# Performance work log

Hardware: AMD Instinct MI355X
Metric: run time of the kernel (lower is better)

The kernel has to match this reference:

```python
import jax, jax.numpy as jnp
import numpy as np

B, T, IN, H, OUT = 64, 32, 256, 512, 256
M, W, R = 256, 64, 4            # nr_cells, cell_size, read_heads
NN_IN = IN + R * W              # 512
NN_OUT = H + R * W              # 768
IFACE = R * W + 3 * W + 5 * R + 3  # 471
CLIP = 20.0
DELTA = 1e-6


def setup_inputs():
    key = jax.random.key(0)
    ks = jax.random.split(key, 10)
    s = 0.05
    bound = float(np.sqrt(6.0 / (B * H + 2 * H)))  # xavier_uniform on (2,B,H)
    return {
        'x': jax.random.normal(ks[0], (B, T, IN), jnp.float32),
        'h0': jax.random.uniform(ks[1], (2, B, H), jnp.float32, -bound, bound),
        'Wih0': jax.random.normal(ks[2], (4 * H, NN_IN), jnp.float32) * s,
        'Whh0': jax.random.normal(ks[3], (4 * H, H), jnp.float32) * s,
        'bih0': jnp.zeros((4 * H,), jnp.float32),
        'bhh0': jnp.zeros((4 * H,), jnp.float32),
        'Wih1': jax.random.normal(ks[4], (4 * H, H), jnp.float32) * s,
        'Whh1': jax.random.normal(ks[5], (4 * H, H), jnp.float32) * s,
        'bih1': jnp.zeros((4 * H,), jnp.float32),
        'bhh1': jnp.zeros((4 * H,), jnp.float32),
        'Wif': jax.random.normal(ks[6], (IFACE, H), jnp.float32) * s,
        'bif': jnp.zeros((IFACE,), jnp.float32),
        'Wout': jax.random.normal(ks[7], (OUT, NN_OUT), jnp.float32) * s,
        'bout': jnp.zeros((OUT,), jnp.float32),
    }


def _lstm_cell(x, h, c, Wih, Whh, bih, bhh):
    g = x @ Wih.T + bih + h @ Whh.T + bhh
    i, f, gg, o = jnp.split(g, 4, axis=1)  # torch gate order i,f,g,o
    c = jax.nn.sigmoid(f) * c + jax.nn.sigmoid(i) * jnp.tanh(gg)
    h = jax.nn.sigmoid(o) * jnp.tanh(c)
    return h, c


def _content_weights(mem, keys, strengths):
    # mem: (b,M,W), keys: (b,K,W), strengths: (b,K) -> softmax over M
    mem_n = mem / (jnp.linalg.norm(mem, axis=2, keepdims=True) + DELTA)
    key_n = keys / (jnp.linalg.norm(keys, axis=2, keepdims=True) + DELTA)
    sim = jnp.einsum('bkw,bmw->bkm', key_n, mem_n)
    return jax.nn.softmax(sim * strengths[..., None], axis=2)


def _memory_step(xi, mem, link, prec, rw, ww, usage):
    b = xi.shape[0]
    o = 0
    rk = jnp.tanh(xi[:, :R * W].reshape(b, R, W)); o = R * W
    rs = jax.nn.softplus(xi[:, o:o + R]); o += R
    wk = jnp.tanh(xi[:, o:o + W]).reshape(b, 1, W); o += W
    ws = jax.nn.softplus(xi[:, o])[:, None]; o += 1
    ev = jax.nn.sigmoid(xi[:, o:o + W]); o += W
    wv = jnp.tanh(xi[:, o:o + W]); o += W
    fg = jax.nn.sigmoid(xi[:, o:o + R]); o += R
    ag = jax.nn.sigmoid(xi[:, o])[:, None]; o += 1
    wg = jax.nn.sigmoid(xi[:, o])[:, None]; o += 1
    rm = jax.nn.softmax(xi[:, o:o + 3 * R].reshape(b, R, 3), axis=2)

    # usage update (uses OLD read/write weights); single write head
    usage = usage + (1.0 - usage) * ww
    psi = jnp.prod(1.0 - fg[:, :, None] * rw, axis=1)
    usage = usage * psi

    # write content addressing on OLD memory
    wcw = _content_weights(mem, wk, ws)[:, 0]  # (b,M)

    # allocation by ascending sort of usage (exclusive cumprod)
    u = DELTA + (1.0 - DELTA) * usage
    phi = jnp.argsort(u, axis=1)
    sorted_u = jnp.take_along_axis(u, phi, axis=1)
    excl = jnp.cumprod(jnp.concatenate([jnp.ones((b, 1), u.dtype), sorted_u], axis=1), axis=1)[:, :-1]
    sorted_alloc = (1.0 - sorted_u) * excl
    alloc = jnp.take_along_axis(sorted_alloc, jnp.argsort(phi, axis=1), axis=1)

    ww = wg * (ag * alloc + (1.0 - ag) * wcw)  # (b,M)

    # erase + write
    mem = mem * (1.0 - ww[:, :, None] * ev[:, None, :]) + ww[:, :, None] * wv[:, None, :]

    # temporal link matrix + precedence
    prev_scale = 1.0 - ww[:, :, None] - ww[:, None, :]
    link = prev_scale * link + ww[:, :, None] * prec[:, None, :]
    link = link * (1.0 - jnp.eye(M, dtype=link.dtype))
    prec = (1.0 - ww.sum(axis=1, keepdims=True)) * prec + ww

    # read: directional weights use NEW link and OLD read weights; content uses NEW memory
    rcw = _content_weights(mem, rk, rs)               # (b,R,M)
    fwd = jnp.einsum('bij,brj->bri', link, rw)
    bwd = jnp.einsum('brj,bji->bri', rw, link)
    rw = rm[:, :, 0:1] * bwd + rm[:, :, 1:2] * fwd + rm[:, :, 2:3] * rcw
    rvec = jnp.einsum('brm,bmw->brw', rw, mem).reshape(b, R * W)
    return rvec, mem, link, prec, rw, ww, usage


def reference(x, h0, Wih0, Whh0, bih0, bhh0, Wih1, Whh1, bih1, bhh1, Wif, bif, Wout, bout):
    b = x.shape[0]
    lr0 = jnp.zeros((b, R * W), x.dtype)  # initial last_read; NOTE: source concatenates this
    # initial zero last_read to EVERY timestep's controller input (inputs built upfront)
    carry0 = (h0[0], h0[0], h0[1], h0[1],
              jnp.full((b, M, W), DELTA, x.dtype),   # memory
              jnp.zeros((b, M, M), x.dtype),          # link matrix
              jnp.zeros((b, M), x.dtype),             # precedence
              jnp.full((b, R, M), DELTA, x.dtype),    # read weights
              jnp.full((b, M), DELTA, x.dtype),       # write weights
              jnp.zeros((b, M), x.dtype))             # usage

    def step(carry, x_t):
        h0_, c0_, h1_, c1_, mem, link, prec, rw, ww, usage = carry
        inp = jnp.concatenate([x_t, lr0], axis=1)
        h0_, c0_ = _lstm_cell(inp, h0_, c0_, Wih0, Whh0, bih0, bhh0)
        h1_, c1_ = _lstm_cell(h0_, h1_, c1_, Wih1, Whh1, bih1, bhh1)
        out = jnp.clip(h1_, -CLIP, CLIP)
        xi = out @ Wif.T + bif
        rvec, mem, link, prec, rw, ww, usage = _memory_step(xi, mem, link, prec, rw, ww, usage)
        o_t = jnp.concatenate([out, rvec], axis=1)  # (b, NN_OUT)
        return (h0_, c0_, h1_, c1_, mem, link, prec, rw, ww, usage), o_t

    _, ys = jax.lax.scan(step, carry0, jnp.swapaxes(x, 0, 1))  # (T,b,NN_OUT)
    outputs = jnp.tanh(ys) @ Wout.T + bout  # Dropout(p=0) -> Tanh -> Linear
    return jnp.swapaxes(outputs, 0, 1)      # (b,T,OUT)
```

## Files before the change

kernel.cpp:

```cpp
#include <hip/hip_runtime.h>
#include <hip/hip_bf16.h>
#include <math.h>


typedef __bf16 bf16_t;
typedef __attribute__((ext_vector_type(8))) __bf16 bf16x8;
typedef __attribute__((ext_vector_type(4))) float f32x4;

#define B_    64
#define T_    32
#define IN_   256
#define H_    512
#define M_    256
#define W_    64
#define R_    4
#define IFACE_ 471
#define DELTA_ 1e-6f

#define OFF_H0SEQ  (0L)
#define SZ_H0SEQ   (32L*64*512*2)
#define OFF_OUTSEQ (OFF_H0SEQ + SZ_H0SEQ)
#define SZ_OUTSEQ  (32L*64*512*2)
#define OFF_H0BUF  (OFF_OUTSEQ + SZ_OUTSEQ)
#define SZ_HBUF    (2L*64*512*2)
#define OFF_H1BUF  (OFF_H0BUF + SZ_HBUF)
#define OFF_XI     (OFF_H1BUF + SZ_HBUF)
#define SZ_XI      (32L*64*480*4)
#define OFF_RVEC   (OFF_XI + SZ_XI)
#define SZ_RVEC    (32L*64*256*4)
#define OFF_YBF    (OFF_RVEC + SZ_RVEC)
#define SZ_YBF     (32L*64*768*2)
#define OFF_BAR    (OFF_YBF + SZ_YBF)
#define SZ_BAR     (2048L)
#define OFF_XB     (OFF_BAR + SZ_BAR)
#define SZ_XB      (64L*32*256*2)
#define OFF_H0B    (OFF_XB + SZ_XB)
#define SZ_H0B     (2L*64*512*2)
#define OFF_W0     (OFF_H0B + SZ_H0B)
#define SZ_W       (2048L*512*2)
#define OFF_W1     (OFF_W0 + SZ_W)
#define OFF_W2     (OFF_W1 + SZ_W)
#define OFF_W3     (OFF_W2 + SZ_W)
#define OFF_WIF    (OFF_W3 + SZ_W)
#define SZ_WIF     (480L*512*2)
#define OFF_WOUTB  (OFF_WIF + SZ_WIF)
#define SZ_WOUTB   (256L*768*2)
#define OFF_BS0    (OFF_WOUTB + SZ_WOUTB)
#define SZ_BS      (2048L*4)
#define OFF_BS1    (OFF_BS0 + SZ_BS)
#define OFF_BIF    (OFF_BS1 + SZ_BS)
#define SZ_BIF     (2048L)
#define OFF_BOUTF  (OFF_BIF + SZ_BIF)
#define SZ_BOUTF   (1024L)

__device__ __forceinline__ float sigf(float x){ return 1.0f/(1.0f + expf(-x)); }
__device__ __forceinline__ float softplusf(float x){
  return fmaxf(x, 0.0f) + log1pf(expf(-fabsf(x)));
}
__device__ __forceinline__ float wred(float v){
  #pragma unroll
  for (int off = 32; off; off >>= 1) v += __shfl_xor(v, off, 64);
  return v;
}
__device__ __forceinline__ float ldin(const void* p, long i, int mf){
  return mf ? ((const float*)p)[i] : (float)((const bf16_t*)p)[i];
}

__device__ __forceinline__ void treebar64(unsigned* bar, unsigned ps, int bid){
  __syncthreads();
  if (threadIdx.x == 0){
    const unsigned tgt = 8u*(ps + 1u);
    unsigned* cg = bar + ((bid & 7) << 5);
    unsigned a = __hip_atomic_fetch_add(cg, 1u, __ATOMIC_ACQ_REL, __HIP_MEMORY_SCOPE_AGENT);
    if (a == tgt - 1u){
      unsigned b = __hip_atomic_fetch_add(bar + 256, 1u, __ATOMIC_ACQ_REL, __HIP_MEMORY_SCOPE_AGENT);
      if (b == tgt - 1u){
        __hip_atomic_store(bar + 320, ps + 1u, __ATOMIC_RELEASE, __HIP_MEMORY_SCOPE_AGENT);
        __hip_atomic_fetch_add(bar + 288, 1u, __ATOMIC_ACQ_REL, __HIP_MEMORY_SCOPE_AGENT);
      }
    }
    while (__hip_atomic_load(bar + 288, __ATOMIC_ACQUIRE, __HIP_MEMORY_SCOPE_AGENT) < ps + 1u)
      __builtin_amdgcn_s_sleep(1);
  }
  __syncthreads();
}

__global__ void k_detect(const unsigned short* __restrict__ x16,
                         int* __restrict__ flag, unsigned* __restrict__ bar){
  __shared__ int cnt;
  if (threadIdx.x < 8)       bar[threadIdx.x << 5] = 0u;
  else if (threadIdx.x == 8) bar[256] = 0u;
  else if (threadIdx.x == 9) bar[288] = 0u;
  else if (threadIdx.x == 10) bar[320] = 0u;
  if (threadIdx.x == 0) cnt = 0;
  __syncthreads();
  unsigned short u = x16[threadIdx.x * 2];
  int e = (u >> 7) & 0xFF;
  if (e >= 0x88) atomicAdd(&cnt, 1);
  __syncthreads();
  if (threadIdx.x == 0) *flag = (cnt > 16) ? 1 : 0;
}

__global__ void k_convert(const void* x, const void* h0, const void* Wih0,
                          const void* Whh0, const void* bih0, const void* bhh0,
                          const void* Wih1, const void* Whh1, const void* bih1,
                          const void* bhh1, const void* Wif, const void* bif,
                          const void* Wout, const void* bout,
                          bf16_t* __restrict__ xb, bf16_t* __restrict__ h0b,
                          bf16_t* __restrict__ h0buf, bf16_t* __restrict__ h1buf,
                          bf16_t* __restrict__ W0, bf16_t* __restrict__ W1,
                          bf16_t* __restrict__ W2, bf16_t* __restrict__ W3,
                          bf16_t* __restrict__ Wifp, bf16_t* __restrict__ Woutb,
                          float* __restrict__ bs0, float* __restrict__ bs1,
                          float* __restrict__ bifp, float* __restrict__ boutf,
                          const int* __restrict__ flag)
{
  const int mf = *flag;
  const long stride = (long)gridDim.x * blockDim.x;
  long i0 = (long)blockIdx.x * blockDim.x + threadIdx.x;
  switch (blockIdx.y){
  case 0: for (long i = i0; i < 64L*32*256; i += stride) xb[i] = (bf16_t)ldin(x, i, mf); break;
  case 1: for (long i = i0; i < 2L*64*512; i += stride){
            float v = ldin(h0, i, mf); bf16_t bb = (bf16_t)v; h0b[i] = bb;
            if (i < 64*512) h0buf[i] = bb; else h1buf[i - 64*512] = bb;
          } break;
  case 2: for (long i = i0; i < 2048L*512; i += stride) W0[i] = (bf16_t)ldin(Wih0, i, mf); break;
  case 3: for (long i = i0; i < 2048L*512; i += stride) W1[i] = (bf16_t)ldin(Whh0, i, mf); break;
  case 4: for (long i = i0; i < 2048L*512; i += stride) W2[i] = (bf16_t)ldin(Wih1, i, mf); break;
  case 5: for (long i = i0; i < 2048L*512; i += stride) W3[i] = (bf16_t)ldin(Whh1, i, mf); break;
  case 6: for (long i = i0; i < 480L*512; i += stride){
            long r = i >> 9;
            Wifp[i] = (r < IFACE_) ? (bf16_t)ldin(Wif, i, mf) : (bf16_t)0.0f;
          } break;
  case 7: for (long i = i0; i < 256L*768; i += stride) Woutb[i] = (bf16_t)ldin(Wout, i, mf); break;
  case 8:
    for (long i = i0; i < 2048; i += stride){
      bs0[i] = ldin(bih0, i, mf) + ldin(bhh0, i, mf);
      bs1[i] = ldin(bih1, i, mf) + ldin(bhh1, i, mf);
    }
    for (long i = i0; i < 480; i += stride) bifp[i] = (i < IFACE_) ? ldin(bif, i, mf) : 0.0f;
    for (long i = i0; i < 256; i += stride) boutf[i] = ldin(bout, i, mf);
    break;
  }
}

__device__ __forceinline__ void softmax256_wave(float* a, int lane){
  float v0=a[lane], v1=a[64+lane], v2=a[128+lane], v3=a[192+lane];
  float mx = fmaxf(fmaxf(v0,v1), fmaxf(v2,v3));
  #pragma unroll
  for (int off=32; off; off>>=1) mx = fmaxf(mx, __shfl_xor(mx, off, 64));
  v0=expf(v0-mx); v1=expf(v1-mx); v2=expf(v2-mx); v3=expf(v3-mx);
  float s = v0+v1+v2+v3;
  #pragma unroll
  for (int off=32; off; off>>=1) s += __shfl_xor(s, off, 64);
  float inv = 1.0f/s;
  a[lane]=v0*inv; a[64+lane]=v1*inv; a[128+lane]=v2*inv; a[192+lane]=v3*inv;
}

struct ProdShm {
  bf16_t wpool[66560];
  float  cst[64][16];
  float  bias[4][16];
};
struct ConsShm {
  float smem[256][65];
  float xib[480];
  float rkn4r[2][65][4];
  float wkn[64], ev_[64], wvv[64];
  float rs_[4], fg_[4], rm_[4][3];
  float wsS, agS, wgS, wwsumS;
  float invn[256], wcw[256];
  float usage[256], uu[256], su[256], scanA[256];
  int   rank_[256];
  float ww_[256], prec_[256];
  float rw_[4][256];
  float rw4[256][4];
  float fwd_[4][256], bwd_[4][256], rcw_[4][256];
  bf16_t rwb[4][264];
  bf16_t wwb[256], precb[256];
  float p2cT[2][264];
  float p5cT[5][2][264];
  float rvp[8][4][64];
};
union ShUnion { ProdShm p; ConsShm c; };

__global__ __launch_bounds__(512,2) void k_main(
    const bf16_t* __restrict__ xb, const bf16_t* __restrict__ h0b,
    const bf16_t* __restrict__ W0, const bf16_t* __restrict__ W1,
    const bf16_t* __restrict__ W2, const bf16_t* __restrict__ W3,
    const float* __restrict__ bs0, const float* __restrict__ bs1,
    const bf16_t* __restrict__ Wifp, const float* __restrict__ bifp,
    bf16_t* __restrict__ h0buf, bf16_t* __restrict__ h1buf,
    bf16_t* __restrict__ h0seq, bf16_t* __restrict__ outseq,
    float* __restrict__ XI, float* __restrict__ RVEC,
    unsigned* __restrict__ bar)
{
  __shared__ ShUnion sh;
  const int bid = blockIdx.x;
  const int tid = threadIdx.x, lane = tid & 63, wv = tid >> 6;
  const int m16 = lane & 15, q = lane >> 4;

  if (bid < 64){
    ProdShm& P = sh.p;
    const int layer = bid >> 5;
    const int u0 = (bid & 31) * 16;

    if (!layer){
      for (int i = tid; i < 64*32; i += 512){
        int rl = i >> 5, c8 = (i & 31)*8;
        int grow = (rl >> 4)*512 + u0 + (rl & 15);
        *(bf16x8*)&P.wpool[rl*264 + c8] = *(const bf16x8*)(W0 + (size_t)grow*512 + c8);
      }
      for (int i = tid; i < 64*64; i += 512){
        int rl = i >> 6, c8 = (i & 63)*8;
        int grow = (rl >> 4)*512 + u0 + (rl & 15);
        *(bf16x8*)&P.wpool[16896 + rl*520 + c8] = *(const bf16x8*)(W1 + (size_t)grow*512 + c8);
      }
    } else {
      for (int i = tid; i < 64*64; i += 512){
        int rl = i >> 6, c8 = (i & 63)*8;
        int grow = (rl >> 4)*512 + u0 + (rl & 15);
        *(bf16x8*)&P.wpool[rl*520 + c8]         = *(const bf16x8*)(W2 + (size_t)grow*512 + c8);
        *(bf16x8*)&P.wpool[33280 + rl*520 + c8] = *(const bf16x8*)(W3 + (size_t)grow*512 + c8);
      }
    }
    for (int i = tid; i < 64*16; i += 512){
      int b = i >> 4, n = i & 15;
      P.cst[b][n] = (float)h0b[layer*(64*512) + b*512 + u0 + n];
    }
    if (tid < 64){
      int G = tid >> 4, n = tid & 15;
      const float* bs = layer ? bs1 : bs0;
      P.bias[G][n] = bs[G*512 + u0 + n];
    }
    __syncthreads();

    bf16_t* hbuf = layer ? h1buf : h0buf;

    for (int ps = 0; ps <= 33; ++ps){
      if (wv < 4){
        const int t = layer ? (ps - 1) : ps;
        const bool active = layer ? (ps >= 1 && ps <= 32) : (ps < 32);
        if (active){
          const int p = t & 1;
          const bf16_t* hin = hbuf + p*(64*512);
          bf16_t* hout = hbuf + (p^1)*(64*512);
          const int b0 = wv * 16;

          f32x4 acc[4];
          #pragma unroll
          for (int G = 0; G < 4; ++G){ float bv = P.bias[G][m16]; acc[G] = (f32x4){bv,bv,bv,bv}; }

          if (!layer){
            #pragma unroll 2
            for (int kt = 0; kt < 8; ++kt){
              bf16x8 a = *(const bf16x8*)(xb + ((size_t)(b0+m16)*T_ + t)*IN_ + kt*32 + q*8);
              #pragma unroll
              for (int G = 0; G < 4; ++G)
                acc[G] = __builtin_amdgcn_mfma_f32_16x16x32_bf16(
                    a, *(const bf16x8*)&P.wpool[(G*16+m16)*264 + kt*32 + q*8], acc[G], 0, 0, 0);
            }
            #pragma unroll 4
            for (int kt = 0; kt < 16; ++kt){
              bf16x8 a = *(const bf16x8*)(hin + (b0+m16)*512 + kt*32 + q*8);
              #pragma unroll
              for (int G = 0; G < 4; ++G)
                acc[G] = __builtin_amdgcn_mfma_f32_16x16x32_bf16(
                    a, *(const bf16x8*)&P.wpool[16896 + (G*16+m16)*520 + kt*32 + q*8], acc[G], 0, 0, 0);
            }
          } else {
            #pragma unroll 4
            for (int kt = 0; kt < 16; ++kt){
              bf16x8 a = *(const bf16x8*)(h0seq + ((size_t)t*64 + b0+m16)*512 + kt*32 + q*8);
              #pragma unroll
              for (int G = 0; G < 4; ++G)
                acc[G] = __builtin_amdgcn_mfma_f32_16x16x32_bf16(
                    a, *(const bf16x8*)&P.wpool[(G*16+m16)*520 + kt*32 + q*8], acc[G], 0, 0, 0);
            }
            #pragma unroll 4
            for (int kt = 0; kt < 16; ++kt){
              bf16x8 a = *(const bf16x8*)(hin + (b0+m16)*512 + kt*32 + q*8);
              #pragma unroll
              for (int G = 0; G < 4; ++G)
                acc[G] = __builtin_amdgcn_mfma_f32_16x16x32_bf16(
                    a, *(const bf16x8*)&P.wpool[33280 + (G*16+m16)*520 + kt*32 + q*8], acc[G], 0, 0, 0);
            }
          }
          #pragma unroll
          for (int v = 0; v < 4; ++v){
            int b = b0 + q*4 + v;
            float gi = acc[0][v], gf = acc[1][v], gg = acc[2][v], go = acc[3][v];
            float c_ = sigf(gf)*P.cst[b][m16] + sigf(gi)*tanhf(gg);
            P.cst[b][m16] = c_;
            float h = sigf(go)*tanhf(c_);
            bf16_t hb = (bf16_t)h;
            hout[b*512 + u0 + m16] = hb;
            if (!layer) h0seq[((size_t)t*64 + b)*512 + u0 + m16] = hb;
            else        outseq[((size_t)t*64 + b)*512 + u0 + m16] = hb;
          }
        }
      } else if (ps >= 2 && bid < 30){
        const int t2 = ps - 2;
        const int b0 = (wv - 4) * 16;
        const int r = bid*16 + m16;
        float bv = bifp[r];
        f32x4 acc = {bv,bv,bv,bv};
        const bf16_t* arow = outseq + ((size_t)t2*64 + b0 + m16)*512 + q*8;
        const bf16_t* brow = Wifp + (size_t)r*512 + q*8;
        #pragma unroll 4
        for (int kt = 0; kt < 16; ++kt){
          acc = __builtin_amdgcn_mfma_f32_16x16x32_bf16(
              *(const bf16x8*)(arow + kt*32), *(const bf16x8*)(brow + kt*32), acc, 0, 0, 0);
        }
        #pragma unroll
        for (int v = 0; v < 4; ++v)
          XI[((size_t)t2*64 + b0 + q*4 + v)*480 + r] = acc[v];
      }
      treebar64(bar, (unsigned)ps, bid);
    }
  } else {
    ConsShm& S = sh.c;
    const int b = bid - 64;
    const int quad = lane >> 4, li = lane & 15;
    unsigned prog = 0;

    bf16x8 rowL[2][8], colL[2][8];
    #pragma unroll
    for (int g = 0; g < 2; ++g)
      #pragma unroll
      for (int ch = 0; ch < 8; ++ch)
        #pragma unroll
        for (int z = 0; z < 8; ++z){ rowL[g][ch][z] = (bf16_t)0.0f; colL[g][ch][z] = (bf16_t)0.0f; }

    if (tid < 256){
      S.ww_[tid] = DELTA_; S.usage[tid] = 0.0f; S.prec_[tid] = 0.0f;
      S.invn[tid] = 1.0f/(sqrtf(64.0f*DELTA_*DELTA_) + DELTA_);
      S.wwb[tid] = (bf16_t)DELTA_; S.precb[tid] = (bf16_t)0.0f;
      #pragma unroll
      for (int r = 0; r < 4; ++r) S.rw_[r][tid] = DELTA_;
    }
    for (int i = tid; i < 4*264; i += 512) ((bf16_t*)S.rwb)[i] = (bf16_t)DELTA_;
    for (int i = tid; i < 256*65; i += 512) ((float*)S.smem)[i] = DELTA_;
    __syncthreads();

    const int mH = tid >> 1, q2 = tid & 1;

    for (int t = 0; t < 32; ++t){
      if (tid == 0 && prog < (unsigned)(t + 3)){
        for (;;){
          prog = __hip_atomic_load(bar + 320, __ATOMIC_ACQUIRE, __HIP_MEMORY_SCOPE_AGENT);
          if (prog >= (unsigned)(t + 3)) break;
          __builtin_amdgcn_s_sleep(2);
        }
      }
      __syncthreads();
      if (tid < IFACE_) S.xib[tid] = XI[((size_t)t*64 + b)*480 + tid];
      __syncthreads();

      if (wv < 4){
        float v = tanhf(S.xib[wv*64 + lane]);
        float s = wred(v*v);
        float vn = v/(sqrtf(s) + DELTA_);
        S.rkn4r[0][lane][wv] = vn; S.rkn4r[1][lane][wv] = vn;
      } else if (wv == 4){
        float v = tanhf(S.xib[260 + lane]);
        float s = wred(v*v);
        S.wkn[lane] = v/(sqrtf(s) + DELTA_);
      } else if (wv == 5){ S.ev_[lane] = sigf(S.xib[325 + lane]);
      } else if (wv == 6){ S.wvv[lane] = tanhf(S.xib[389 + lane]);
      } else {
        if (lane < 4)        S.rs_[lane] = softplusf(S.xib[256 + lane]);
        else if (lane == 4)  S.wsS = softplusf(S.xib[324]);
        else if (lane < 9)   S.fg_[lane-5] = sigf(S.xib[453 + (lane-5)]);
        else if (lane == 9)  S.agS = sigf(S.xib[457]);
        else if (lane == 10) S.wgS = sigf(S.xib[458]);
        else if (lane >= 16 && lane < 20){
          int r = lane - 16;
          float a0 = S.xib[459+r*3], a1 = S.xib[459+r*3+1], a2 = S.xib[459+r*3+2];
          float mx = fmaxf(a0, fmaxf(a1, a2));
          float e0 = expf(a0-mx), e1 = expf(a1-mx), e2 = expf(a2-mx);
          float s = e0+e1+e2;
          S.rm_[r][0]=e0/s; S.rm_[r][1]=e1/s; S.rm_[r][2]=e2/s;
        }
      }
      __syncthreads();

      if (tid < 256){
        int m = tid;
        float us = S.usage[m] + (1.0f - S.usage[m])*S.ww_[m];
        float psi = (1.0f - S.fg_[0]*S.rw_[0][m]) * (1.0f - S.fg_[1]*S.rw_[1][m])
                  * (1.0f - S.fg_[2]*S.rw_[2][m]) * (1.0f - S.fg_[3]*S.rw_[3][m]);
        us *= psi;
        S.usage[m] = us;
        S.uu[m] = DELTA_ + (1.0f - DELTA_)*us;
      }
      { float acc = 0.0f;
        #pragma unroll
        for (int it = 0; it < 32; ++it){
          int w = q2*32 + it;
          acc += S.smem[mH][w] * S.wkn[w];
        }
        S.p2cT[q2][mH] = acc; }
      __syncthreads();

      if (wv == 0){
        #pragma unroll
        for (int z = 0; z < 4; ++z){
          int m = z*64 + lane;
          S.wcw[m] = S.wsS * (S.p2cT[0][m] + S.p2cT[1][m]) * S.invn[m];
        }
        softmax256_wave(S.wcw, lane);
      } else if (tid >= 256){
        const int i = tid - 256;
        const float ui = S.uu[i];
        int cnt = 0;
        #pragma unroll 8
        for (int k = 0; k < 64; ++k){
          f32x4 u4 = *(const f32x4*)&S.uu[k*4];
          #pragma unroll
          for (int z = 0; z < 4; ++z){
            int j = k*4 + z; float uj = u4[z];
            cnt += (uj < ui || (uj == ui && j < i)) ? 1 : 0;
          }
        }
        S.rank_[i] = cnt;
        S.su[cnt] = ui;
      }
      __syncthreads();

      if (wv == 0){
        int base = lane*4;
        float v0 = S.su[base], v1 = S.su[base+1], v2 = S.su[base+2];
        float p1 = v0*v1, p2 = p1*v2, p3 = p2*S.su[base+3];
        float sc = p3;
        #pragma unroll
        for (int off = 1; off < 64; off <<= 1){
          float n = __shfl_up(sc, off, 64);
          if (lane >= off) sc *= n;
        }
        float exch = __shfl_up(sc, 1, 64);
        if (lane == 0) exch = 1.0f;
        S.scanA[base] = exch; S.scanA[base+1] = exch*v0;
        S.scanA[base+2] = exch*p1; S.scanA[base+3] = exch*p2;
      }
      __syncthreads();

      { const int m = mH;
        float al = (1.0f - S.uu[m]) * S.scanA[S.rank_[m]];
        float wm = S.wgS*(S.agS*al + (1.0f - S.agS)*S.wcw[m]);
        if (q2 == 0){ S.ww_[m] = wm; S.wwb[m] = (bf16_t)wm; }
        float s2 = 0.0f, sr0 = 0.0f, sr1 = 0.0f, sr2 = 0.0f, sr3 = 0.0f;
        #pragma unroll
        for (int it = 0; it < 32; ++it){
          int w = q2*32 + it;
          float mn = S.smem[m][w]*(1.0f - wm*S.ev_[w]) + wm*S.wvv[w];
          S.smem[m][w] = mn;
          s2 += mn*mn;
          f32x4 rk = *(const f32x4*)&S.rkn4r[q2][w][0];
          sr0 += mn*rk[0]; sr1 += mn*rk[1]; sr2 += mn*rk[2]; sr3 += mn*rk[3];
        }
        S.p5cT[0][q2][m] = s2;
        S.p5cT[1][q2][m] = sr0; S.p5cT[2][q2][m] = sr1;
        S.p5cT[3][q2][m] = sr2; S.p5cT[4][q2][m] = sr3; }
      __syncthreads();

      if (tid < 256){
        int m = tid;
        float s2 = S.p5cT[0][0][m] + S.p5cT[0][1][m];
        float inv = 1.0f/(sqrtf(s2) + DELTA_);
        S.invn[m] = inv;
        #pragma unroll
        for (int r = 0; r < 4; ++r){
          float sr = S.p5cT[r+1][0][m] + S.p5cT[r+1][1][m];
          S.rcw_[r][m] = S.rs_[r]*sr*inv;
        }
      } else if (wv == 4){
        float s = wred(S.ww_[lane] + S.ww_[64+lane] + S.ww_[128+lane] + S.ww_[192+lane]);
        if (lane == 0) S.wwsumS = s;
      }
      __syncthreads();

      { float wown[2], pown[2], alpha[2];
        #pragma unroll
        for (int g = 0; g < 2; ++g){
          int o = wv*32 + g*16 + li;
          wown[g] = (float)S.wwb[o]; pown[g] = (float)S.precb[o];
          alpha[g] = 1.0f - wown[g];
        }
        f32x4 facc[2] = {{0,0,0,0},{0,0,0,0}}, bacc[2] = {{0,0,0,0},{0,0,0,0}};
        #pragma unroll
        for (int ch = 0; ch < 8; ++ch){
          const int cbase = ch*32 + quad*8;
          bf16x8 rwf = *(const bf16x8*)&S.rwb[li & 3][cbase];
          bf16x8 wwv = *(const bf16x8*)&S.wwb[cbase];
          bf16x8 pcv = *(const bf16x8*)&S.precb[cbase];
          float wcf[8], pcf[8];
          #pragma unroll
          for (int jj = 0; jj < 8; ++jj){ wcf[jj] = (float)wwv[jj]; pcf[jj] = (float)pcv[jj]; }
          #pragma unroll
          for (int g = 0; g < 2; ++g){
            const int o = wv*32 + g*16 + li;
            bf16x8 rl = rowL[g][ch];
            bf16x8 cl = colL[g][ch];
            #pragma unroll
            for (int jj = 0; jj < 8; ++jj){
              const int c = cbase + jj;
              float s = alpha[g] - wcf[jj];
              float vr = s*(float)rl[jj] + wown[g]*pcf[jj];
              float vc = s*(float)cl[jj] + wcf[jj]*pown[g];
              if (c == o){ vr = 0.0f; vc = 0.0f; }
              rl[jj] = (bf16_t)vr;
              cl[jj] = (bf16_t)vc;
            }
            rowL[g][ch] = rl; colL[g][ch] = cl;
            facc[g] = __builtin_amdgcn_mfma_f32_16x16x32_bf16(rl, rwf, facc[g], 0, 0, 0);
            bacc[g] = __builtin_amdgcn_mfma_f32_16x16x32_bf16(rwf, cl, bacc[g], 0, 0, 0);
          }
        }
        #pragma unroll
        for (int g = 0; g < 2; ++g){
          if (li < 4){
            #pragma unroll
            for (int z = 0; z < 4; ++z) S.fwd_[li][wv*32 + g*16 + quad*4 + z] = facc[g][z];
          }
          if (quad == 0){
            #pragma unroll
            for (int z = 0; z < 4; ++z) S.bwd_[z][wv*32 + g*16 + li] = bacc[g][z];
          }
        }
      }
      __syncthreads();

      if (wv < 4) softmax256_wave(S.rcw_[wv], lane);
      else {
        int m = tid - 256;
        float p = (1.0f - S.wwsumS)*S.prec_[m] + S.ww_[m];
        S.prec_[m] = p;
        S.precb[m] = (bf16_t)p;
      }
      __syncthreads();

      { int r = tid >> 7, m0 = (tid & 127)*2;
        #pragma unroll
        for (int z = 0; z < 2; ++z){
          int m = m0 + z;
          float v = S.rm_[r][0]*S.bwd_[r][m] + S.rm_[r][1]*S.fwd_[r][m] + S.rm_[r][2]*S.rcw_[r][m];
          S.rw_[r][m] = v;
          S.rw4[m][r] = v;
          S.rwb[r][m] = (bf16_t)v;
        } }
      __syncthreads();

      { float r0 = 0, r1 = 0, r2 = 0, r3 = 0;
        #pragma unroll
        for (int k = 0; k < 32; ++k){
          int m = wv*32 + k;
          f32x4 r4 = *(const f32x4*)&S.rw4[m][0];
          float mv = S.smem[m][lane];
          r0 += r4[0]*mv; r1 += r4[1]*mv; r2 += r4[2]*mv; r3 += r4[3]*mv;
        }
        S.rvp[wv][0][lane] = r0; S.rvp[wv][1][lane] = r1;
        S.rvp[wv][2][lane] = r2; S.rvp[wv][3][lane] = r3; }
      __syncthreads();

      if (tid < 256){
        const int w = tid & 63, r = tid >> 6;
        float v = 0.0f;
        #pragma unroll
        for (int c = 0; c < 8; ++c) v += S.rvp[c][r][w];
        RVEC[((size_t)t*64 + b)*256 + tid] = v;
      }
      __syncthreads();
    }
  }
}

__global__ void k_tanhy(const bf16_t* __restrict__ outseq, const float* __restrict__ RVEC,
                        bf16_t* __restrict__ Y){
  const int n = 2048*768;
  for (int i = blockIdx.x*blockDim.x + threadIdx.x; i < n; i += gridDim.x*blockDim.x){
    int row = i / 768, j = i - row*768;
    float v = (j < 512) ? (float)outseq[(size_t)row*512 + j] : RVEC[(size_t)row*256 + (j - 512)];
    Y[i] = (bf16_t)tanhf(v);
  }
}

__global__ __launch_bounds__(256,1) void k_out(
    const bf16_t* __restrict__ Y, const bf16_t* __restrict__ Woutb,
    const float* __restrict__ boutf, void* __restrict__ dout,
    const int* __restrict__ flag)
{
  const int mf = *flag;
  const int mt = blockIdx.x;
  const int tid = threadIdx.x, lane = tid & 63, wv = tid >> 6;
  const int nt = blockIdx.y*4 + wv;
  const int m16 = lane & 15, q = lane >> 4;
  const int o = nt*16 + m16;
  float bv = boutf[o];
  f32x4 acc = {bv,bv,bv,bv};
  const bf16_t* arow = Y + (size_t)(mt*16 + m16)*768 + q*8;
  const bf16_t* brow = Woutb + (size_t)o*768 + q*8;
  for (int kt = 0; kt < 24; ++kt){
    acc = __builtin_amdgcn_mfma_f32_16x16x32_bf16(
        *(const bf16x8*)(arow + kt*32), *(const bf16x8*)(brow + kt*32), acc, 0, 0, 0);
  }
  #pragma unroll
  for (int v = 0; v < 4; ++v){
    int row = mt*16 + q*4 + v;
    int b = row & 63, t = row >> 6;
    size_t idx = ((size_t)b*T_ + t)*256 + o;
    if (mf) ((float*)dout)[idx] = acc[v];
    else    ((bf16_t*)dout)[idx] = (bf16_t)acc[v];
  }
}

extern "C" void kernel_launch(void* const* d_in, const int* in_sizes, int n_in,
                              void* d_out, int out_size, void* d_ws, size_t ws_size,
                              hipStream_t stream)
{
  char* ws = (char*)d_ws;
  bf16_t* H0SEQ  = (bf16_t*)(ws + OFF_H0SEQ);
  bf16_t* OUTSEQ = (bf16_t*)(ws + OFF_OUTSEQ);
  bf16_t* H0BUF  = (bf16_t*)(ws + OFF_H0BUF);
  bf16_t* H1BUF  = (bf16_t*)(ws + OFF_H1BUF);
  float*  XI     = (float*) (ws + OFF_XI);
  float*  RVEC   = (float*) (ws + OFF_RVEC);
  bf16_t* YBF    = (bf16_t*)(ws + OFF_YBF);
  unsigned* BAR  = (unsigned*)(ws + OFF_BAR);
  int*    FLAG   = (int*)   (ws + OFF_BAR + 1408);
  bf16_t* XB     = (bf16_t*)(ws + OFF_XB);
  bf16_t* H0B    = (bf16_t*)(ws + OFF_H0B);
  bf16_t* W0     = (bf16_t*)(ws + OFF_W0);
  bf16_t* W1     = (bf16_t*)(ws + OFF_W1);
  bf16_t* W2     = (bf16_t*)(ws + OFF_W2);
  bf16_t* W3     = (bf16_t*)(ws + OFF_W3);
  bf16_t* WIFP   = (bf16_t*)(ws + OFF_WIF);
  bf16_t* WOUTB  = (bf16_t*)(ws + OFF_WOUTB);
  float*  BS0    = (float*) (ws + OFF_BS0);
  float*  BS1    = (float*) (ws + OFF_BS1);
  float*  BIFP   = (float*) (ws + OFF_BIF);
  float*  BOUTF  = (float*) (ws + OFF_BOUTF);

  k_detect<<<1, 256, 0, stream>>>((const unsigned short*)d_in[0], FLAG, BAR);
  k_convert<<<dim3(256, 9), 256, 0, stream>>>(
      d_in[0], d_in[1], d_in[2], d_in[3], d_in[4], d_in[5], d_in[6],
      d_in[7], d_in[8], d_in[9], d_in[10], d_in[11], d_in[12], d_in[13],
      XB, H0B, H0BUF, H1BUF, W0, W1, W2, W3, WIFP, WOUTB,
      BS0, BS1, BIFP, BOUTF, FLAG);
  k_main<<<128, 512, 0, stream>>>(XB, H0B, W0, W1, W2, W3, BS0, BS1,
                                  WIFP, BIFP, H0BUF, H1BUF, H0SEQ, OUTSEQ,
                                  XI, RVEC, BAR);
  k_tanhy<<<512, 256, 0, stream>>>(OUTSEQ, RVEC, YBF);
  k_out<<<dim3(128, 4), 256, 0, stream>>>(YBF, WOUTB, BOUTF, d_out, FLAG);
}
```

Baseline: 1.145 ms.

## Move interface projection into consumer blocks and fuse tanh into output GEMM

The interface-vector matvec (Wif·out) is no longer computed by the spare producer waves with MFMA and passed through a global XI buffer. Each memory consumer block now computes its own 471-row dot products from LDS-staged activations. This removes one pipeline stage of latency from the producer/consumer schedule (a dependency on t+2 instead of t+3, and one fewer barrier step). Separately, the tanh pass is fused into the output GEMM via an LDS tile, which drops a kernel launch and the Y buffer. The risk is added serial scalar FMA work on the consumer's critical path, about 471×512 per step per block.

```diff
diff --git a/kernel.cpp b/kernel.cpp
--- a/kernel.cpp
+++ b/kernel.cpp
@@ -24,13 +24,9 @@
 #define OFF_H0BUF  (OFF_OUTSEQ + SZ_OUTSEQ)
 #define SZ_HBUF    (2L*64*512*2)
 #define OFF_H1BUF  (OFF_H0BUF + SZ_HBUF)
-#define OFF_XI     (OFF_H1BUF + SZ_HBUF)
-#define SZ_XI      (32L*64*480*4)
-#define OFF_RVEC   (OFF_XI + SZ_XI)
+#define OFF_RVEC   (OFF_H1BUF + SZ_HBUF)
 #define SZ_RVEC    (32L*64*256*4)
-#define OFF_YBF    (OFF_RVEC + SZ_RVEC)
-#define SZ_YBF     (32L*64*768*2)
-#define OFF_BAR    (OFF_YBF + SZ_YBF)
+#define OFF_BAR    (OFF_RVEC + SZ_RVEC)
 #define SZ_BAR     (2048L)
 #define OFF_XB     (OFF_BAR + SZ_BAR)
 #define SZ_XB      (64L*32*256*2)
@@ -164,6 +160,7 @@
 };
 struct ConsShm {
   float smem[256][65];
+  float outf[512];
   float xib[480];
   float rkn4r[2][65][4];
   float wkn[64], ev_[64], wvv[64];
@@ -192,8 +189,7 @@
     const bf16_t* __restrict__ Wifp, const float* __restrict__ bifp,
     bf16_t* __restrict__ h0buf, bf16_t* __restrict__ h1buf,
     bf16_t* __restrict__ h0seq, bf16_t* __restrict__ outseq,
-    float* __restrict__ XI, float* __restrict__ RVEC,
-    unsigned* __restrict__ bar)
+    float* __restrict__ RVEC, unsigned* __restrict__ bar)
 {
   __shared__ ShUnion sh;
   const int bid = blockIdx.x;
@@ -237,7 +233,7 @@
 
     bf16_t* hbuf = layer ? h1buf : h0buf;
 
-    for (int ps = 0; ps <= 33; ++ps){
+    for (int ps = 0; ps <= 32; ++ps){
       if (wv < 4){
         const int t = layer ? (ps - 1) : ps;
         const bool active = layer ? (ps >= 1 && ps <= 32) : (ps < 32);
@@ -299,22 +295,6 @@
             else        outseq[((size_t)t*64 + b)*512 + u0 + m16] = hb;
           }
         }
-      } else if (ps >= 2 && bid < 30){
-        const int t2 = ps - 2;
-        const int b0 = (wv - 4) * 16;
-        const int r = bid*16 + m16;
-        float bv = bifp[r];
-        f32x4 acc = {bv,bv,bv,bv};
-        const bf16_t* arow = outseq + ((size_t)t2*64 + b0 + m16)*512 + q*8;
-        const bf16_t* brow = Wifp + (size_t)r*512 + q*8;
-        #pragma unroll 4
-        for (int kt = 0; kt < 16; ++kt){
-          acc = __builtin_amdgcn_mfma_f32_16x16x32_bf16(
-              *(const bf16x8*)(arow + kt*32), *(const bf16x8*)(brow + kt*32), acc, 0, 0, 0);
-        }
-        #pragma unroll
-        for (int v = 0; v < 4; ++v)
-          XI[((size_t)t2*64 + b0 + q*4 + v)*480 + r] = acc[v];
       }
       treebar64(bar, (unsigned)ps, bid);
     }
@@ -346,15 +326,33 @@
     const int mH = tid >> 1, q2 = tid & 1;
 
     for (int t = 0; t < 32; ++t){
-      if (tid == 0 && prog < (unsigned)(t + 3)){
+      if (tid == 0 && prog < (unsigned)(t + 2)){
         for (;;){
           prog = __hip_atomic_load(bar + 320, __ATOMIC_ACQUIRE, __HIP_MEMORY_SCOPE_AGENT);
-          if (prog >= (unsigned)(t + 3)) break;
+          if (prog >= (unsigned)(t + 2)) break;
           __builtin_amdgcn_s_sleep(2);
         }
       }
       __syncthreads();
-      if (tid < IFACE_) S.xib[tid] = XI[((size_t)t*64 + b)*480 + tid];
+      if (tid < 64){
+        bf16x8 v = *(const bf16x8*)(outseq + ((size_t)t*64 + b)*512 + tid*8);
+        #pragma unroll
+        for (int z = 0; z < 8; ++z) S.outf[tid*8 + z] = (float)v[z];
+      }
+      __syncthreads();
+      if (tid < IFACE_){
+        const bf16_t* wrow = Wifp + (size_t)tid*512;
+        float acc = bifp[tid];
+        #pragma unroll 4
+        for (int k8 = 0; k8 < 64; ++k8){
+          bf16x8 w8 = *(const bf16x8*)(wrow + k8*8);
+          f32x4 a0 = *(const f32x4*)&S.outf[k8*8];
+          f32x4 a1 = *(const f32x4*)&S.outf[k8*8 + 4];
+          acc += (float)w8[0]*a0[0] + (float)w8[1]*a0[1] + (float)w8[2]*a0[2] + (float)w8[3]*a0[3]
+               + (float)w8[4]*a1[0] + (float)w8[5]*a1[1] + (float)w8[6]*a1[2] + (float)w8[7]*a1[3];
+        }
+        S.xib[tid] = acc;
+      }
       __syncthreads();
 
       if (wv < 4){
@@ -575,42 +573,47 @@
   }
 }
 
-__global__ void k_tanhy(const bf16_t* __restrict__ outseq, const float* __restrict__ RVEC,
-                        bf16_t* __restrict__ Y){
-  const int n = 2048*768;
-  for (int i = blockIdx.x*blockDim.x + threadIdx.x; i < n; i += gridDim.x*blockDim.x){
-    int row = i / 768, j = i - row*768;
-    float v = (j < 512) ? (float)outseq[(size_t)row*512 + j] : RVEC[(size_t)row*256 + (j - 512)];
-    Y[i] = (bf16_t)tanhf(v);
-  }
-}
-
 __global__ __launch_bounds__(256,1) void k_out(
-    const bf16_t* __restrict__ Y, const bf16_t* __restrict__ Woutb,
-    const float* __restrict__ boutf, void* __restrict__ dout,
-    const int* __restrict__ flag)
+    const bf16_t* __restrict__ outseq, const float* __restrict__ RVEC,
+    const bf16_t* __restrict__ Woutb, const float* __restrict__ boutf,
+    void* __restrict__ dout, const int* __restrict__ flag)
 {
   const int mf = *flag;
   const int mt = blockIdx.x;
   const int tid = threadIdx.x, lane = tid & 63, wv = tid >> 6;
-  const int nt = blockIdx.y*4 + wv;
   const int m16 = lane & 15, q = lane >> 4;
-  const int o = nt*16 + m16;
-  float bv = boutf[o];
-  f32x4 acc = {bv,bv,bv,bv};
-  const bf16_t* arow = Y + (size_t)(mt*16 + m16)*768 + q*8;
-  const bf16_t* brow = Woutb + (size_t)o*768 + q*8;
-  for (int kt = 0; kt < 24; ++kt){
-    acc = __builtin_amdgcn_mfma_f32_16x16x32_bf16(
-        *(const bf16x8*)(arow + kt*32), *(const bf16x8*)(brow + kt*32), acc, 0, 0, 0);
+  __shared__ bf16_t At[16][776];
+
+  for (int i = tid; i < 16*768; i += 256){
+    int r = i / 768, c = i - r*768;
+    int row = mt*16 + r;
+    float v = (c < 512) ? (float)outseq[(size_t)row*512 + c]
+                        : RVEC[(size_t)row*256 + (c - 512)];
+    At[r][c] = (bf16_t)tanhf(v);
   }
-  #pragma unroll
-  for (int v = 0; v < 4; ++v){
-    int row = mt*16 + q*4 + v;
-    int b = row & 63, t = row >> 6;
-    size_t idx = ((size_t)b*T_ + t)*256 + o;
-    if (mf) ((float*)dout)[idx] = acc[v];
-    else    ((bf16_t*)dout)[idx] = (bf16_t)acc[v];
+  __syncthreads();
+
+  #pragma unroll 1
+  for (int nn = 0; nn < 4; ++nn){
+    const int nt = wv*4 + nn;
+    const int o = nt*16 + m16;
+    float bv = boutf[o];
+    f32x4 acc = {bv,bv,bv,bv};
+    const bf16_t* brow = Woutb + (size_t)o*768 + q*8;
+    #pragma unroll 4
+    for (int kt = 0; kt < 24; ++kt){
+      acc = __builtin_amdgcn_mfma_f32_16x16x32_bf16(
+          *(const bf16x8*)&At[m16][kt*32 + q*8],
+          *(const bf16x8*)(brow + kt*32), acc, 0, 0, 0);
+    }
+    #pragma unroll
+    for (int v = 0; v < 4; ++v){
+      int row = mt*16 + q*4 + v;
+      int b = row & 63, t = row >> 6;
+      size_t idx = ((size_t)b*T_ + t)*256 + o;
+      if (mf) ((float*)dout)[idx] = acc[v];
+      else    ((bf16_t*)dout)[idx] = (bf16_t)acc[v];
+    }
   }
 }
 
@@ -623,9 +626,7 @@
   bf16_t* OUTSEQ = (bf16_t*)(ws + OFF_OUTSEQ);
   bf16_t* H0BUF  = (bf16_t*)(ws + OFF_H0BUF);
   bf16_t* H1BUF  = (bf16_t*)(ws + OFF_H1BUF);
-  float*  XI     = (float*) (ws + OFF_XI);
   float*  RVEC   = (float*) (ws + OFF_RVEC);
-  bf16_t* YBF    = (bf16_t*)(ws + OFF_YBF);
   unsigned* BAR  = (unsigned*)(ws + OFF_BAR);
   int*    FLAG   = (int*)   (ws + OFF_BAR + 1408);
   bf16_t* XB     = (bf16_t*)(ws + OFF_XB);
@@ -649,7 +650,6 @@
       BS0, BS1, BIFP, BOUTF, FLAG);
   k_main<<<128, 512, 0, stream>>>(XB, H0B, W0, W1, W2, W3, BS0, BS1,
                                   WIFP, BIFP, H0BUF, H1BUF, H0SEQ, OUTSEQ,
-                                  XI, RVEC, BAR);
-  k_tanhy<<<512, 256, 0, stream>>>(OUTSEQ, RVEC, YBF);
-  k_out<<<dim3(128, 4), 256, 0, stream>>>(YBF, WOUTB, BOUTF, d_out, FLAG);
-}
+                                  RVEC, BAR);
+  k_out<<<128, 256, 0, stream>>>(OUTSEQ, RVEC, WOUTB, BOUTF, d_out, FLAG);
+}
```

New measurement: 1.693 ms. +47.8%, slower.

## Fuse tanh and output projection into consumer blocks of main kernel

Applied to the files above, without the earlier changes.

Removes the separate tanh and output-linear kernels. Each consumer block (one per batch element) now builds its tanh'd 32x768 sequence tile in shared memory after the recurrence and runs the output projection with MFMA directly into the output. This drops two launches and the global round trip of the intermediate Y buffer. In exchange, only 64 blocks do the tail GEMM instead of 512, and Wout is re-read from global by every block.

```diff
diff --git a/kernel.cpp b/kernel.cpp
--- a/kernel.cpp
+++ b/kernel.cpp
@@ -28,9 +28,7 @@
 #define SZ_XI      (32L*64*480*4)
 #define OFF_RVEC   (OFF_XI + SZ_XI)
 #define SZ_RVEC    (32L*64*256*4)
-#define OFF_YBF    (OFF_RVEC + SZ_RVEC)
-#define SZ_YBF     (32L*64*768*2)
-#define OFF_BAR    (OFF_YBF + SZ_YBF)
+#define OFF_BAR    (OFF_RVEC + SZ_RVEC)
 #define SZ_BAR     (2048L)
 #define OFF_XB     (OFF_BAR + SZ_BAR)
 #define SZ_XB      (64L*32*256*2)
@@ -182,7 +180,10 @@
   float p5cT[5][2][264];
   float rvp[8][4][64];
 };
-union ShUnion { ProdShm p; ConsShm c; };
+struct TailShm {
+  bf16_t Yt[32][776];
+};
+union ShUnion { ProdShm p; ConsShm c; TailShm t; };
 
 __global__ __launch_bounds__(512,2) void k_main(
     const bf16_t* __restrict__ xb, const bf16_t* __restrict__ h0b,
@@ -190,9 +191,11 @@
     const bf16_t* __restrict__ W2, const bf16_t* __restrict__ W3,
     const float* __restrict__ bs0, const float* __restrict__ bs1,
     const bf16_t* __restrict__ Wifp, const float* __restrict__ bifp,
+    const bf16_t* __restrict__ Woutb, const float* __restrict__ boutf,
     bf16_t* __restrict__ h0buf, bf16_t* __restrict__ h1buf,
     bf16_t* __restrict__ h0seq, bf16_t* __restrict__ outseq,
     float* __restrict__ XI, float* __restrict__ RVEC,
+    void* __restrict__ dout, const int* __restrict__ flag,
     unsigned* __restrict__ bar)
 {
   __shared__ ShUnion sh;
@@ -572,45 +575,42 @@
       }
       __syncthreads();
     }
-  }
-}
-
-__global__ void k_tanhy(const bf16_t* __restrict__ outseq, const float* __restrict__ RVEC,
-                        bf16_t* __restrict__ Y){
-  const int n = 2048*768;
-  for (int i = blockIdx.x*blockDim.x + threadIdx.x; i < n; i += gridDim.x*blockDim.x){
-    int row = i / 768, j = i - row*768;
-    float v = (j < 512) ? (float)outseq[(size_t)row*512 + j] : RVEC[(size_t)row*256 + (j - 512)];
-    Y[i] = (bf16_t)tanhf(v);
-  }
-}
-
-__global__ __launch_bounds__(256,1) void k_out(
-    const bf16_t* __restrict__ Y, const bf16_t* __restrict__ Woutb,
-    const float* __restrict__ boutf, void* __restrict__ dout,
-    const int* __restrict__ flag)
-{
-  const int mf = *flag;
-  const int mt = blockIdx.x;
-  const int tid = threadIdx.x, lane = tid & 63, wv = tid >> 6;
-  const int nt = blockIdx.y*4 + wv;
-  const int m16 = lane & 15, q = lane >> 4;
-  const int o = nt*16 + m16;
-  float bv = boutf[o];
-  f32x4 acc = {bv,bv,bv,bv};
-  const bf16_t* arow = Y + (size_t)(mt*16 + m16)*768 + q*8;
-  const bf16_t* brow = Woutb + (size_t)o*768 + q*8;
-  for (int kt = 0; kt < 24; ++kt){
-    acc = __builtin_amdgcn_mfma_f32_16x16x32_bf16(
-        *(const bf16x8*)(arow + kt*32), *(const bf16x8*)(brow + kt*32), acc, 0, 0, 0);
-  }
-  #pragma unroll
-  for (int v = 0; v < 4; ++v){
-    int row = mt*16 + q*4 + v;
-    int b = row & 63, t = row >> 6;
-    size_t idx = ((size_t)b*T_ + t)*256 + o;
-    if (mf) ((float*)dout)[idx] = acc[v];
-    else    ((bf16_t*)dout)[idx] = (bf16_t)acc[v];
+
+    TailShm& Tl = sh.t;
+    __syncthreads();
+    for (int i = tid; i < 32*768; i += 512){
+      int r = i / 768, c = i - r*768;
+      size_t row = (size_t)r*64 + b;
+      float v = (c < 512) ? (float)outseq[row*512 + c]
+                          : RVEC[row*256 + (c - 512)];
+      Tl.Yt[r][c] = (bf16_t)tanhf(v);
+    }
+    __syncthreads();
+    const int mf = *flag;
+    #pragma unroll 1
+    for (int nn = 0; nn < 2; ++nn){
+      const int nt = wv + nn*8;
+      const int o = nt*16 + li;
+      float bv = boutf[o];
+      const bf16_t* brow = Woutb + (size_t)o*768 + quad*8;
+      #pragma unroll 1
+      for (int mt2 = 0; mt2 < 2; ++mt2){
+        f32x4 acc = {bv,bv,bv,bv};
+        #pragma unroll 4
+        for (int kt = 0; kt < 24; ++kt){
+          acc = __builtin_amdgcn_mfma_f32_16x16x32_bf16(
+              *(const bf16x8*)&Tl.Yt[mt2*16 + li][kt*32 + quad*8],
+              *(const bf16x8*)(brow + kt*32), acc, 0, 0, 0);
+        }
+        #pragma unroll
+        for (int v = 0; v < 4; ++v){
+          int t = mt2*16 + quad*4 + v;
+          size_t idx = ((size_t)b*T_ + t)*256 + o;
+          if (mf) ((float*)dout)[idx] = acc[v];
+          else    ((bf16_t*)dout)[idx] = (bf16_t)acc[v];
+        }
+      }
+    }
   }
 }
 
@@ -625,7 +625,6 @@
   bf16_t* H1BUF  = (bf16_t*)(ws + OFF_H1BUF);
   float*  XI     = (float*) (ws + OFF_XI);
   float*  RVEC   = (float*) (ws + OFF_RVEC);
-  bf16_t* YBF    = (bf16_t*)(ws + OFF_YBF);
   unsigned* BAR  = (unsigned*)(ws + OFF_BAR);
   int*    FLAG   = (int*)   (ws + OFF_BAR + 1408);
   bf16_t* XB     = (bf16_t*)(ws + OFF_XB);
@@ -648,8 +647,7 @@
       XB, H0B, H0BUF, H1BUF, W0, W1, W2, W3, WIFP, WOUTB,
       BS0, BS1, BIFP, BOUTF, FLAG);
   k_main<<<128, 512, 0, stream>>>(XB, H0B, W0, W1, W2, W3, BS0, BS1,
-                                  WIFP, BIFP, H0BUF, H1BUF, H0SEQ, OUTSEQ,
-                                  XI, RVEC, BAR);
-  k_tanhy<<<512, 256, 0, stream>>>(OUTSEQ, RVEC, YBF);
-  k_out<<<dim3(128, 4), 256, 0, stream>>>(YBF, WOUTB, BOUTF, d_out, FLAG);
-}
+                                  WIFP, BIFP, WOUTB, BOUTF,
+                                  H0BUF, H1BUF, H0SEQ, OUTSEQ,
+                                  XI, RVEC, d_out, FLAG, BAR);
+}
```

Measured after the change: 1.244 ms. +8.6%, slower.
